# Optimization experiments

Hardware: AMD Instinct MI355X
Metric: run time of the kernel (lower is better)

Reference implementation:

```python
import jax, jax.numpy as jnp
import numpy as np

N_NODES = 100000
N_EDGES = 1600000
D = 128


def sage_conv(x, src, dst, W_l, b_l, W_r):
    # mean aggregation of neighbor features: messages flow src -> dst
    msgs = x[src]                                           # [E, D] gather
    agg = jax.ops.segment_sum(msgs, dst, num_segments=x.shape[0])  # [N, D]
    deg = jax.ops.segment_sum(jnp.ones((src.shape[0],), x.dtype), dst,
                              num_segments=x.shape[0])       # [N]
    agg = agg / jnp.maximum(deg, 1.0)[:, None]
    # PyG SAGEConv: lin_l(aggregated) + lin_r(root); bias lives in lin_l
    return agg @ W_l.T + b_l + x @ W_r.T


def setup_inputs() -> dict:
    key = jax.random.key(0)
    ks = jax.random.split(key, 8)
    s = 1.0 / np.sqrt(D)
    return {
        "x": jax.random.normal(ks[0], (N_NODES, D), dtype=jnp.float32),
        "edge_index": jax.random.randint(ks[1], (2, N_EDGES), 0, N_NODES, dtype=jnp.int64),
        "W1_l": jax.random.normal(ks[2], (D, D), dtype=jnp.float32) * s,
        "b1": jnp.zeros((D,), dtype=jnp.float32),
        "W1_r": jax.random.normal(ks[3], (D, D), dtype=jnp.float32) * s,
        "W2_l": jax.random.normal(ks[4], (D, D), dtype=jnp.float32) * s,
        "b2": jnp.zeros((D,), dtype=jnp.float32),
        "W2_r": jax.random.normal(ks[5], (D, D), dtype=jnp.float32) * s,
    }


def reference(x, edge_index, W1_l, b1, W1_r, W2_l, b2, W2_r):
    src, dst = edge_index[0], edge_index[1]
    h = jax.nn.relu(sage_conv(x, src, dst, W1_l, b1, W1_r))
    out = sage_conv(h, src, dst, W2_l, b2, W2_r)
    return out
```

## Files before the change

### kernel.cpp

```cpp
#include <hip/hip_runtime.h>
#include <cstdint>
#include <cstddef>

#define D 128

typedef unsigned short ushort_t;
typedef unsigned int uint_t;
typedef __attribute__((ext_vector_type(8))) short bf16x8;
typedef __attribute__((ext_vector_type(4))) float f32x4;

static __device__ __forceinline__ unsigned short f2bf(float f) {
    unsigned int u = __float_as_uint(f);
    u = (u + 0x7FFFu + ((u >> 16) & 1u)) >> 16;
    return (unsigned short)u;
}
static __device__ __forceinline__ float bf_lo(uint_t v) {
    return __uint_as_float(v << 16);
}
static __device__ __forceinline__ float bf_hi(uint_t v) {
    return __uint_as_float(v & 0xFFFF0000u);
}


__global__ __launch_bounds__(256) void bkt_hist(const int* __restrict__ dst,
                                                int* __restrict__ bhist, int E) {
    __shared__ int lh[512];
    int t = threadIdx.x;
    lh[t] = 0;
    lh[t + 256] = 0;
    __syncthreads();
    int base = blockIdx.x * 4096;
#pragma unroll
    for (int i = 0; i < 16; ++i) {
        int e = base + i * 256 + t;
        if (e < E) atomicAdd(&lh[dst[e] >> 8], 1);
    }
    __syncthreads();
    if (lh[t]) atomicAdd(&bhist[t], lh[t]);
    if (lh[t + 256]) atomicAdd(&bhist[t + 256], lh[t + 256]);
}

__global__ __launch_bounds__(512) void bkt_scan(const int* __restrict__ bhist,
                                                int* __restrict__ boff,
                                                int* __restrict__ bcur,
                                                int* __restrict__ row_ptr,
                                                int N, int E) {
    __shared__ int s[512];
    int t = threadIdx.x;
    int v = bhist[t];
    s[t] = v;
    __syncthreads();
    for (int off = 1; off < 512; off <<= 1) {
        int u = (t >= off) ? s[t - off] : 0;
        __syncthreads();
        s[t] += u;
        __syncthreads();
    }
    int ex = s[t] - v;
    boff[t] = ex;
    bcur[t] = ex;
    if (t == 511) boff[512] = s[511];
    if (t == 0) row_ptr[N] = E;
}

__global__ __launch_bounds__(256) void bkt_scatter(const int* __restrict__ src,
                                                   const int* __restrict__ dst,
                                                   int* __restrict__ bcur,
                                                   int* __restrict__ ebuf, int E) {
    __shared__ int lh[512];
    __shared__ int gb[512];
    int t = threadIdx.x;
    lh[t] = 0;
    lh[t + 256] = 0;
    __syncthreads();
    int base = blockIdx.x * 4096;
    unsigned pk[16];
#pragma unroll
    for (int i = 0; i < 16; ++i) {
        int e = base + i * 256 + t;
        unsigned p = 0xFFFFFFFFu;
        if (e < E) {
            int d = dst[e];
            int bkt = d >> 8;
            int r = atomicAdd(&lh[bkt], 1);
            p = ((unsigned)r << 17) | ((unsigned)bkt << 8) | (unsigned)(d & 255);
        }
        pk[i] = p;
    }
    __syncthreads();
    if (lh[t]) gb[t] = atomicAdd(&bcur[t], lh[t]);
    if (lh[t + 256]) gb[t + 256] = atomicAdd(&bcur[t + 256], lh[t + 256]);
    __syncthreads();
#pragma unroll
    for (int i = 0; i < 16; ++i) {
        int e = base + i * 256 + t;
        if (e < E) {
            unsigned p = pk[i];
            int bkt = (p >> 8) & 511;
            int r = (int)(p >> 17);
            ebuf[gb[bkt] + r] = src[e] | ((int)(p & 255) << 20);
        }
    }
}

__global__ __launch_bounds__(256) void bkt_build(const int* __restrict__ ebuf,
                                                 const int* __restrict__ boff,
                                                 int* __restrict__ row_ptr,
                                                 int* __restrict__ csr, int N) {
    __shared__ int lcnt[256];
    __shared__ int lofs[256];
    __shared__ int lcur[256];
    int t = threadIdx.x;
    int b = blockIdx.x;
    int base = b << 8;
    int ebeg = boff[b], eend = boff[b + 1];
    lcnt[t] = 0;
    __syncthreads();
    for (int e = ebeg + t; e < eend; e += 256)
        atomicAdd(&lcnt[((unsigned)ebuf[e]) >> 20], 1);
    __syncthreads();
    int v = lcnt[t];
    lofs[t] = v;
    __syncthreads();
    for (int off = 1; off < 256; off <<= 1) {
        int u = (t >= off) ? lofs[t - off] : 0;
        __syncthreads();
        lofs[t] += u;
        __syncthreads();
    }
    int ex = lofs[t] - v;
    __syncthreads();
    lofs[t] = ex;
    lcur[t] = 0;
    if (base + t < N) row_ptr[base + t] = ebeg + ex;
    __syncthreads();
    for (int e = ebeg + t; e < eend; e += 256) {
        int u = ebuf[e];
        int d = ((unsigned)u) >> 20;
        int r = atomicAdd(&lcur[d], 1);
        csr[ebeg + lofs[d] + r] = u & 0xFFFFF;
    }
}


__global__ __launch_bounds__(256) void cast_x_kernel(const float* __restrict__ src,
                                                     ushort_t* __restrict__ dst,
                                                     long n) {
    long i = ((long)blockIdx.x * 256 + threadIdx.x) * 8;
    if (i >= n) return;
    float4 a = *(const float4*)(src + i);
    float4 b = *(const float4*)(src + i + 4);
    uint4 o;
    o.x = (uint_t)f2bf(a.x) | ((uint_t)f2bf(a.y) << 16);
    o.y = (uint_t)f2bf(a.z) | ((uint_t)f2bf(a.w) << 16);
    o.z = (uint_t)f2bf(b.x) | ((uint_t)f2bf(b.y) << 16);
    o.w = (uint_t)f2bf(b.z) | ((uint_t)f2bf(b.w) << 16);
    *(uint4*)(dst + i) = o;
}

__global__ __launch_bounds__(256) void cast_w_kernel(const float* __restrict__ s0,
                                                     const float* __restrict__ s1,
                                                     const float* __restrict__ s2,
                                                     const float* __restrict__ s3,
                                                     ushort_t* __restrict__ d0,
                                                     ushort_t* __restrict__ d1,
                                                     ushort_t* __restrict__ d2,
                                                     ushort_t* __restrict__ d3) {
    const float* s = (blockIdx.y == 0) ? s0 : (blockIdx.y == 1) ? s1
                   : (blockIdx.y == 2) ? s2 : s3;
    ushort_t* d = (blockIdx.y == 0) ? d0 : (blockIdx.y == 1) ? d1
                : (blockIdx.y == 2) ? d2 : d3;
    long i = ((long)blockIdx.x * 256 + threadIdx.x) * 8;
    float4 a = *(const float4*)(s + i);
    float4 b = *(const float4*)(s + i + 4);
    uint4 o;
    o.x = (uint_t)f2bf(a.x) | ((uint_t)f2bf(a.y) << 16);
    o.y = (uint_t)f2bf(a.z) | ((uint_t)f2bf(a.w) << 16);
    o.z = (uint_t)f2bf(b.x) | ((uint_t)f2bf(b.y) << 16);
    o.w = (uint_t)f2bf(b.z) | ((uint_t)f2bf(b.w) << 16);
    *(uint4*)(d + i) = o;
}


static __device__ __forceinline__ void acc8(uint4 v, float a[8]) {
    a[0] += bf_lo(v.x); a[1] += bf_hi(v.x);
    a[2] += bf_lo(v.y); a[3] += bf_hi(v.y);
    a[4] += bf_lo(v.z); a[5] += bf_hi(v.z);
    a[6] += bf_lo(v.w); a[7] += bf_hi(v.w);
}

static __device__ __forceinline__ uint4 grow(const ushort_t* __restrict__ xin,
                                             int s, int l16) {
    unsigned off = ((unsigned)s << 8) | ((unsigned)l16 << 4);
    return *(const uint4*)((const char*)xin + off);
}

__global__ __launch_bounds__(256) void agg_b_kernel(const ushort_t* __restrict__ xin,
                                                    const int* __restrict__ csr,
                                                    const int* __restrict__ row_ptr,
                                                    ushort_t* __restrict__ aggb, int N) {
    int node = blockIdx.x * 4 + (threadIdx.x >> 6);
    if (node >= N) return;
    int lane = threadIdx.x & 63;
    int g = lane >> 4;
    int l16 = lane & 15;
    int beg = row_ptr[node], end = row_ptr[node + 1];
    int deg = end - beg;
    float a[8] = {0.f, 0.f, 0.f, 0.f, 0.f, 0.f, 0.f, 0.f};

    if (deg > 0) {
        int deg64 = min(deg, 64);
        int myidx = csr[beg + min(lane, deg - 1)];
        int e = 0;
        for (; e + 16 <= deg64; e += 16) {
            int s0 = __shfl(myidx, e + g);
            int s1 = __shfl(myidx, e + 4 + g);
            int s2 = __shfl(myidx, e + 8 + g);
            int s3 = __shfl(myidx, e + 12 + g);
            uint4 v0 = grow(xin, s0, l16);
            uint4 v1 = grow(xin, s1, l16);
            uint4 v2 = grow(xin, s2, l16);
            uint4 v3 = grow(xin, s3, l16);
            acc8(v0, a); acc8(v1, a); acc8(v2, a); acc8(v3, a);
        }
        if (e + 8 <= deg64) {
            int s0 = __shfl(myidx, e + g);
            int s1 = __shfl(myidx, e + 4 + g);
            uint4 v0 = grow(xin, s0, l16);
            uint4 v1 = grow(xin, s1, l16);
            acc8(v0, a); acc8(v1, a);
            e += 8;
        }
        for (; e < deg64; e += 4) {
            int ee = min(e + g, deg64 - 1);
            int s = __shfl(myidx, ee);
            uint4 v = grow(xin, s, l16);
            if (e + g < deg64) acc8(v, a);
        }
        for (int e2 = 64; e2 < deg; e2 += 4) {
            int s = csr[beg + min(e2 + g, deg - 1)];
            uint4 v = grow(xin, s, l16);
            if (e2 + g < deg) acc8(v, a);
        }
    }

#pragma unroll
    for (int i = 0; i < 8; ++i) {
        a[i] += __shfl_xor(a[i], 16);
        a[i] += __shfl_xor(a[i], 32);
    }
    if (g == 0) {
        float inv = 1.0f / fmaxf((float)deg, 1.0f);
        uint4 o;
        o.x = (uint_t)f2bf(a[0] * inv) | ((uint_t)f2bf(a[1] * inv) << 16);
        o.y = (uint_t)f2bf(a[2] * inv) | ((uint_t)f2bf(a[3] * inv) << 16);
        o.z = (uint_t)f2bf(a[4] * inv) | ((uint_t)f2bf(a[5] * inv) << 16);
        o.w = (uint_t)f2bf(a[6] * inv) | ((uint_t)f2bf(a[7] * inv) << 16);
        unsigned off = ((unsigned)node << 8) | ((unsigned)l16 << 4);
        *(uint4*)((char*)aggb + off) = o;
    }
}


__global__ __launch_bounds__(256) void gemm_mfma(const ushort_t* __restrict__ Aagg,
                                                 const ushort_t* __restrict__ Ax,
                                                 const ushort_t* __restrict__ Wl,
                                                 const ushort_t* __restrict__ Wr,
                                                 const float* __restrict__ bias,
                                                 ushort_t* __restrict__ out_bf,
                                                 float* __restrict__ out_f32,
                                                 int N, int relu_bf) {
    __shared__ ushort_t sA[128 * 32];
    __shared__ ushort_t sW[128 * 32];
    int tid = threadIdx.x;
    int wave = tid >> 6, lane = tid & 63;
    int quad = lane >> 4, l15 = lane & 15;
    int wm = wave & 1, wc = wave >> 1;
    int n0 = blockIdx.x * 128;

    int sr = tid >> 2;
    int sseg = (tid & 3) * 8;

    f32x4 acc[4][4];
#pragma unroll
    for (int mt = 0; mt < 4; ++mt)
#pragma unroll
        for (int nt = 0; nt < 4; ++nt) acc[mt][nt] = (f32x4){0.f, 0.f, 0.f, 0.f};

    int ga0 = min(n0 + sr, N - 1);
    int ga1 = min(n0 + sr + 64, N - 1);

#pragma unroll
    for (int c = 0; c < 8; ++c) {
        const ushort_t* Ab = (c < 4) ? Aagg : Ax;
        const ushort_t* Wb = (c < 4) ? Wl : Wr;
        int koff = (c & 3) * 32 + sseg;
        bf16x8 va0 = *(const bf16x8*)(Ab + (size_t)ga0 * D + koff);
        bf16x8 va1 = *(const bf16x8*)(Ab + (size_t)ga1 * D + koff);
        bf16x8 vw0 = *(const bf16x8*)(Wb + (size_t)sr * D + koff);
        bf16x8 vw1 = *(const bf16x8*)(Wb + (size_t)(sr + 64) * D + koff);
        __syncthreads();
        *(bf16x8*)&sA[sr * 32 + sseg] = va0;
        *(bf16x8*)&sA[(sr + 64) * 32 + sseg] = va1;
        *(bf16x8*)&sW[sr * 32 + sseg] = vw0;
        *(bf16x8*)&sW[(sr + 64) * 32 + sseg] = vw1;
        __syncthreads();

        bf16x8 af[4], wf[4];
#pragma unroll
        for (int mt = 0; mt < 4; ++mt)
            af[mt] = *(const bf16x8*)&sA[(wm * 64 + mt * 16 + l15) * 32 + quad * 8];
#pragma unroll
        for (int nt = 0; nt < 4; ++nt)
            wf[nt] = *(const bf16x8*)&sW[(wc * 64 + nt * 16 + l15) * 32 + quad * 8];
#pragma unroll
        for (int mt = 0; mt < 4; ++mt)
#pragma unroll
            for (int nt = 0; nt < 4; ++nt)
                acc[mt][nt] = __builtin_amdgcn_mfma_f32_16x16x32_bf16(
                    af[mt], wf[nt], acc[mt][nt], 0, 0, 0);
    }

#pragma unroll
    for (int mt = 0; mt < 4; ++mt) {
#pragma unroll
        for (int nt = 0; nt < 4; ++nt) {
            int col = wc * 64 + nt * 16 + l15;
            float bv = bias[col];
#pragma unroll
            for (int reg = 0; reg < 4; ++reg) {
                int row = n0 + wm * 64 + mt * 16 + quad * 4 + reg;
                if (row < N) {
                    float v = acc[mt][nt][reg] + bv;
                    if (relu_bf) {
                        v = fmaxf(v, 0.f);
                        out_bf[(size_t)row * D + col] = f2bf(v);
                    } else {
                        out_f32[(size_t)row * D + col] = v;
                    }
                }
            }
        }
    }
}


extern "C" void kernel_launch(void* const* d_in, const int* in_sizes, int n_in,
                              void* d_out, int out_size, void* d_ws, size_t ws_size,
                              hipStream_t stream) {
    const float* x   = (const float*)d_in[0];
    const int*   ei  = (const int*)d_in[1];
    const float* W1l = (const float*)d_in[2];
    const float* b1  = (const float*)d_in[3];
    const float* W1r = (const float*)d_in[4];
    const float* W2l = (const float*)d_in[5];
    const float* b2  = (const float*)d_in[6];
    const float* W2r = (const float*)d_in[7];
    float* out = (float*)d_out;

    int N = in_sizes[0] / D;
    int E = in_sizes[1] / 2;
    const int* src = ei;
    const int* dst = ei + E;

    char* ws = (char*)d_ws;
    size_t off = 0;
    auto take = [&](size_t bytes) -> char* {
        char* p = ws + off;
        off += (bytes + 255) & ~(size_t)255;
        return p;
    };
    int*      row_ptr = (int*)take((size_t)(N + 1) * sizeof(int));
    int*      bhist   = (int*)take((size_t)(512 + 512 + 513) * sizeof(int));
    int*      bcur    = bhist + 512;
    int*      boff    = bhist + 1024;
    int*      ebuf    = (int*)take((size_t)E * sizeof(int));
    int*      csr     = (int*)take((size_t)E * sizeof(int));
    ushort_t* xb      = (ushort_t*)take((size_t)N * D * sizeof(ushort_t));
    ushort_t* hb      = (ushort_t*)take((size_t)N * D * sizeof(ushort_t));
    ushort_t* aggb    = (ushort_t*)take((size_t)N * D * sizeof(ushort_t));
    ushort_t* W1lb    = (ushort_t*)take((size_t)D * D * sizeof(ushort_t));
    ushort_t* W1rb    = (ushort_t*)take((size_t)D * D * sizeof(ushort_t));
    ushort_t* W2lb    = (ushort_t*)take((size_t)D * D * sizeof(ushort_t));
    ushort_t* W2rb    = (ushort_t*)take((size_t)D * D * sizeof(ushort_t));
    (void)ws_size;
    (void)n_in;
    (void)out_size;

    hipMemsetAsync(bhist, 0, 1024 * sizeof(int), stream);

    int NB = (N + 255) / 256;
    int EB = (E + 4095) / 4096;

    bkt_hist<<<EB, 256, 0, stream>>>(dst, bhist, E);
    bkt_scan<<<1, 512, 0, stream>>>(bhist, boff, bcur, row_ptr, N, E);
    bkt_scatter<<<EB, 256, 0, stream>>>(src, dst, bcur, ebuf, E);
    bkt_build<<<NB, 256, 0, stream>>>(ebuf, boff, row_ptr, csr, N);

    long nx = (long)N * D;
    cast_x_kernel<<<(int)((nx / 8 + 255) / 256), 256, 0, stream>>>(x, xb, nx);
    cast_w_kernel<<<dim3(8, 4), 256, 0, stream>>>(W1l, W1r, W2l, W2r,
                                                  W1lb, W1rb, W2lb, W2rb);

    int ablocks = (N + 3) / 4;
    int gblocks = (N + 127) / 128;

    agg_b_kernel<<<ablocks, 256, 0, stream>>>(xb, csr, row_ptr, aggb, N);
    gemm_mfma<<<gblocks, 256, 0, stream>>>(aggb, xb, W1lb, W1rb, b1, hb, nullptr, N, 1);

    agg_b_kernel<<<ablocks, 256, 0, stream>>>(hb, csr, row_ptr, aggb, N);
    gemm_mfma<<<gblocks, 256, 0, stream>>>(aggb, hb, W2lb, W2rb, b2, nullptr, out, N, 0);
}
```

Measured before the change: 335.0 us.

## Fuse histogram and casts into one launch, stage scatter in LDS, split agg tail

Merges the bucket histogram, the x cast and the weight casts into a single front kernel that dispatches on block index, removing two launches. The bucket scatter now sorts each block's edges by bucket in shared memory through a local prefix scan before writing them out, so global writes to ebuf land in contiguous runs instead of scattering. The aggregation kernel's remainder loop is replaced by one unmasked 4-edge step plus a single masked step. In exchange the scatter uses much more LDS per block (about 28 KB), which can lower its occupancy.

```diff
diff --git a/kernel.cpp b/kernel.cpp
--- a/kernel.cpp
+++ b/kernel.cpp
@@ -21,24 +21,56 @@
     return __uint_as_float(v & 0xFFFF0000u);
 }
 
-
-__global__ __launch_bounds__(256) void bkt_hist(const int* __restrict__ dst,
-                                                int* __restrict__ bhist, int E) {
+static __device__ __forceinline__ void cast8(const float* __restrict__ s,
+                                             ushort_t* __restrict__ d) {
+    float4 a = *(const float4*)s;
+    float4 b = *(const float4*)(s + 4);
+    uint4 o;
+    o.x = (uint_t)f2bf(a.x) | ((uint_t)f2bf(a.y) << 16);
+    o.y = (uint_t)f2bf(a.z) | ((uint_t)f2bf(a.w) << 16);
+    o.z = (uint_t)f2bf(b.x) | ((uint_t)f2bf(b.y) << 16);
+    o.w = (uint_t)f2bf(b.z) | ((uint_t)f2bf(b.w) << 16);
+    *(uint4*)d = o;
+}
+
+
+__global__ __launch_bounds__(256) void front_fused(
+    const int* __restrict__ dst, int* __restrict__ bhist, int E, int EB,
+    const float* __restrict__ x, ushort_t* __restrict__ xb, long nx, int CX,
+    const float* __restrict__ W1l, const float* __restrict__ W1r,
+    const float* __restrict__ W2l, const float* __restrict__ W2r,
+    ushort_t* __restrict__ W1lb, ushort_t* __restrict__ W1rb,
+    ushort_t* __restrict__ W2lb, ushort_t* __restrict__ W2rb) {
     __shared__ int lh[512];
-    int t = threadIdx.x;
-    lh[t] = 0;
-    lh[t + 256] = 0;
-    __syncthreads();
-    int base = blockIdx.x * 4096;
-#pragma unroll
-    for (int i = 0; i < 16; ++i) {
-        int e = base + i * 256 + t;
-        if (e < E) atomicAdd(&lh[dst[e] >> 8], 1);
-    }
-    __syncthreads();
-    if (lh[t]) atomicAdd(&bhist[t], lh[t]);
-    if (lh[t + 256]) atomicAdd(&bhist[t + 256], lh[t + 256]);
-}
+    int b = blockIdx.x, t = threadIdx.x;
+    if (b < EB) {
+        lh[t] = 0;
+        lh[t + 256] = 0;
+        __syncthreads();
+        int base = b * 4096;
+#pragma unroll
+        for (int i = 0; i < 16; ++i) {
+            int e = base + i * 256 + t;
+            if (e < E) atomicAdd(&lh[dst[e] >> 8], 1);
+        }
+        __syncthreads();
+        if (lh[t]) atomicAdd(&bhist[t], lh[t]);
+        if (lh[t + 256]) atomicAdd(&bhist[t + 256], lh[t + 256]);
+    } else if (b < EB + CX) {
+        long i = ((long)(b - EB) * 256 + t) * 8;
+        if (i < nx) cast8(x + i, xb + i);
+    } else {
+        int bb = b - EB - CX;
+        int arr = bb >> 3;
+        long i = ((long)(bb & 7) * 256 + t) * 8;
+        const float* s = (arr == 0) ? W1l : (arr == 1) ? W1r
+                       : (arr == 2) ? W2l : W2r;
+        ushort_t* d = (arr == 0) ? W1lb : (arr == 1) ? W1rb
+                    : (arr == 2) ? W2lb : W2rb;
+        cast8(s + i, d + i);
+    }
+}
+
 
 __global__ __launch_bounds__(512) void bkt_scan(const int* __restrict__ bhist,
                                                 int* __restrict__ boff,
@@ -68,7 +100,10 @@
                                                    int* __restrict__ bcur,
                                                    int* __restrict__ ebuf, int E) {
     __shared__ int lh[512];
+    __shared__ int lofs[512];
     __shared__ int gb[512];
+    __shared__ int sv[4096];
+    __shared__ unsigned short sb[4096];
     int t = threadIdx.x;
     lh[t] = 0;
     lh[t + 256] = 0;
@@ -88,8 +123,23 @@
         pk[i] = p;
     }
     __syncthreads();
-    if (lh[t]) gb[t] = atomicAdd(&bcur[t], lh[t]);
-    if (lh[t + 256]) gb[t + 256] = atomicAdd(&bcur[t + 256], lh[t + 256]);
+    int a0 = lh[2 * t], a1 = lh[2 * t + 1];
+    int ps = a0 + a1;
+    gb[t] = ps;
+    __syncthreads();
+    for (int off = 1; off < 256; off <<= 1) {
+        int u = (t >= off) ? gb[t - off] : 0;
+        __syncthreads();
+        gb[t] += u;
+        __syncthreads();
+    }
+    int inc = gb[t];
+    int exb = inc - ps;
+    __syncthreads();
+    lofs[2 * t] = exb;
+    lofs[2 * t + 1] = exb + a0;
+    if (a0) gb[2 * t] = atomicAdd(&bcur[2 * t], a0);
+    if (a1) gb[2 * t + 1] = atomicAdd(&bcur[2 * t + 1], a1);
     __syncthreads();
 #pragma unroll
     for (int i = 0; i < 16; ++i) {
@@ -98,8 +148,16 @@
             unsigned p = pk[i];
             int bkt = (p >> 8) & 511;
             int r = (int)(p >> 17);
-            ebuf[gb[bkt] + r] = src[e] | ((int)(p & 255) << 20);
-        }
+            int pos = lofs[bkt] + r;
+            sv[pos] = src[e] | ((int)(p & 255) << 20);
+            sb[pos] = (unsigned short)bkt;
+        }
+    }
+    __syncthreads();
+    int cnt = min(E - base, 4096);
+    for (int i = t; i < cnt; i += 256) {
+        int b2 = sb[i];
+        ebuf[gb[b2] + (i - lofs[b2])] = sv[i];
     }
 }
 
@@ -140,45 +198,6 @@
         int r = atomicAdd(&lcur[d], 1);
         csr[ebeg + lofs[d] + r] = u & 0xFFFFF;
     }
-}
-
-
-__global__ __launch_bounds__(256) void cast_x_kernel(const float* __restrict__ src,
-                                                     ushort_t* __restrict__ dst,
-                                                     long n) {
-    long i = ((long)blockIdx.x * 256 + threadIdx.x) * 8;
-    if (i >= n) return;
-    float4 a = *(const float4*)(src + i);
-    float4 b = *(const float4*)(src + i + 4);
-    uint4 o;
-    o.x = (uint_t)f2bf(a.x) | ((uint_t)f2bf(a.y) << 16);
-    o.y = (uint_t)f2bf(a.z) | ((uint_t)f2bf(a.w) << 16);
-    o.z = (uint_t)f2bf(b.x) | ((uint_t)f2bf(b.y) << 16);
-    o.w = (uint_t)f2bf(b.z) | ((uint_t)f2bf(b.w) << 16);
-    *(uint4*)(dst + i) = o;
-}
-
-__global__ __launch_bounds__(256) void cast_w_kernel(const float* __restrict__ s0,
-                                                     const float* __restrict__ s1,
-                                                     const float* __restrict__ s2,
-                                                     const float* __restrict__ s3,
-                                                     ushort_t* __restrict__ d0,
-                                                     ushort_t* __restrict__ d1,
-                                                     ushort_t* __restrict__ d2,
-                                                     ushort_t* __restrict__ d3) {
-    const float* s = (blockIdx.y == 0) ? s0 : (blockIdx.y == 1) ? s1
-                   : (blockIdx.y == 2) ? s2 : s3;
-    ushort_t* d = (blockIdx.y == 0) ? d0 : (blockIdx.y == 1) ? d1
-                : (blockIdx.y == 2) ? d2 : d3;
-    long i = ((long)blockIdx.x * 256 + threadIdx.x) * 8;
-    float4 a = *(const float4*)(s + i);
-    float4 b = *(const float4*)(s + i + 4);
-    uint4 o;
-    o.x = (uint_t)f2bf(a.x) | ((uint_t)f2bf(a.y) << 16);
-    o.y = (uint_t)f2bf(a.z) | ((uint_t)f2bf(a.w) << 16);
-    o.z = (uint_t)f2bf(b.x) | ((uint_t)f2bf(b.y) << 16);
-    o.w = (uint_t)f2bf(b.z) | ((uint_t)f2bf(b.w) << 16);
-    *(uint4*)(d + i) = o;
 }
 
 
@@ -231,7 +250,13 @@
             acc8(v0, a); acc8(v1, a);
             e += 8;
         }
-        for (; e < deg64; e += 4) {
+        if (e + 4 <= deg64) {
+            int s0 = __shfl(myidx, e + g);
+            uint4 v0 = grow(xin, s0, l16);
+            acc8(v0, a);
+            e += 4;
+        }
+        if (e < deg64) {
             int ee = min(e + g, deg64 - 1);
             int s = __shfl(myidx, ee);
             uint4 v = grow(xin, s, l16);
@@ -277,7 +302,6 @@
     int quad = lane >> 4, l15 = lane & 15;
     int wm = wave & 1, wc = wave >> 1;
     int n0 = blockIdx.x * 128;
-
     int sr = tid >> 2;
     int sseg = (tid & 3) * 8;
 
@@ -391,17 +415,16 @@
 
     int NB = (N + 255) / 256;
     int EB = (E + 4095) / 4096;
-
-    bkt_hist<<<EB, 256, 0, stream>>>(dst, bhist, E);
+    long nx = (long)N * D;
+    int CX = (int)((nx / 8 + 255) / 256);
+
+    front_fused<<<EB + CX + 32, 256, 0, stream>>>(
+        dst, bhist, E, EB, x, xb, nx, CX,
+        W1l, W1r, W2l, W2r, W1lb, W1rb, W2lb, W2rb);
     bkt_scan<<<1, 512, 0, stream>>>(bhist, boff, bcur, row_ptr, N, E);
     bkt_scatter<<<EB, 256, 0, stream>>>(src, dst, bcur, ebuf, E);
     bkt_build<<<NB, 256, 0, stream>>>(ebuf, boff, row_ptr, csr, N);
 
-    long nx = (long)N * D;
-    cast_x_kernel<<<(int)((nx / 8 + 255) / 256), 256, 0, stream>>>(x, xb, nx);
-    cast_w_kernel<<<dim3(8, 4), 256, 0, stream>>>(W1l, W1r, W2l, W2r,
-                                                  W1lb, W1rb, W2lb, W2rb);
-
     int ablocks = (N + 3) / 4;
     int gblocks = (N + 127) / 128;
 
```

Result: no change. 336.4 us (+0.4%).
